# Kernel optimization log

Measured on AMD Instinct MI355X. Metric: run time of the kernel, lower is better.

## Reference

```python
import jax, jax.numpy as jnp
import numpy as np

SEG = 4  # segments


def setup_inputs() -> dict:
    key = jax.random.key(0)
    k1, k2, k3, k4 = jax.random.split(key, 4)
    B, C, H, W_ = 8, 64, 512, 512
    O = 64
    x = jax.random.normal(k1, (B, C, H, W_), dtype=jnp.float32)
    W = jax.random.normal(k2, (O, C), dtype=jnp.float32) * 0.05   # Linear weight [out, in]
    b = jax.random.normal(k3, (O,), dtype=jnp.float32) * 0.05
    seg_w = jax.random.normal(k4, (SEG, SEG), dtype=jnp.float32) * 0.1
    return {"x": x, "W": W, "b": b, "seg_w": seg_w}


def reference(x, W, b, seg_w):
    B, C, H, Wd = x.shape
    S = SEG
    hs, ws = H // S, Wd // S
    # segment mean-pool: [B, C, S, hs, S, ws] -> [B, C, S, S]
    pooled = x.reshape(B, C, S, hs, S, ws).mean(axis=(3, 5))
    # small linear per segment tile: [B, O, S, S]
    t = jnp.einsum('bcij,oc->boij', pooled, W) + b[None, :, None, None]
    weighted = t * seg_w[None, None, :, :]
    # broadcast each tile value back over its hs x ws block
    out = jnp.broadcast_to(
        weighted[:, :, :, None, :, None], (B, W.shape[0], S, hs, S, ws)
    ).reshape(B, W.shape[0], H, Wd)
    return out
```

## Files before the change

kernel.cpp:

```cpp
#include <hip/hip_runtime.h>

#define B_   8
#define C_   64
#define O_   64
#define H_   512
#define Wd_  512
#define SEG_ 4
#define HS_  128
#define WS_  128

__global__ __launch_bounds__(256) void pool_kernel(const float* __restrict__ x,
                                                   float* __restrict__ pooled) {
    const int blk = blockIdx.x;
    const int i   = blk & 3;
    const int bc  = blk >> 2;
    const float4* base =
        (const float4*)(x + ((size_t)bc * H_ + (size_t)i * HS_) * Wd_);

    const int tid = threadIdx.x;
    float sum = 0.f;
    #pragma unroll 8
    for (int f = tid; f < HS_ * Wd_ / 4; f += 256) {
        float4 v = base[f];
        sum += (v.x + v.y) + (v.z + v.w);
    }

    for (int off = 16; off >= 1; off >>= 1)
        sum += __shfl_down(sum, off, 32);

    __shared__ float sums[8];
    const int g = tid >> 5;
    if ((tid & 31) == 0) sums[g] = sum;
    __syncthreads();

    if (tid < 4) {
        float total = sums[tid] + sums[tid + 4];
        pooled[(size_t)blk * 4 + tid] = total * (1.0f / (HS_ * WS_));
    }
}

__global__ __launch_bounds__(256) void linear_kernel(const float* __restrict__ pooled,
                                                     const float* __restrict__ Wm,
                                                     const float* __restrict__ bias,
                                                     const float* __restrict__ seg_w,
                                                     float* __restrict__ weighted) {
    const int idx = blockIdx.x * 256 + threadIdx.x;
    if (idx >= B_ * O_ * 16) return;
    const int ij = idx & 15;
    const int o  = (idx >> 4) & (O_ - 1);
    const int b  = idx >> 10;

    const float* pp = pooled + (size_t)b * C_ * 16 + ij;
    const float* wr = Wm + (size_t)o * C_;
    float acc = 0.f;
    #pragma unroll 16
    for (int c = 0; c < C_; ++c)
        acc += pp[c * 16] * wr[c];

    weighted[idx] = (acc + bias[o]) * seg_w[ij];
}

__global__ __launch_bounds__(256) void bcast_kernel(const float* __restrict__ weighted,
                                                    float* __restrict__ out) {
    const int blk = blockIdx.x;
    const int i   = blk & 3;
    const int bo  = blk >> 2;
    const float* wv = weighted + (size_t)bo * 16 + (size_t)i * 4;

    const int tid = threadIdx.x;
    const int j   = (tid & 127) >> 5;
    const float v = wv[j];
    const float4 vv = make_float4(v, v, v, v);

    float4* base = (float4*)(out + ((size_t)bo * H_ + (size_t)i * HS_) * Wd_);
    #pragma unroll 8
    for (int f = tid; f < HS_ * Wd_ / 4; f += 256)
        base[f] = vv;
}

extern "C" void kernel_launch(void* const* d_in, const int* in_sizes, int n_in,
                              void* d_out, int out_size, void* d_ws, size_t ws_size,
                              hipStream_t stream) {
    const float* x     = (const float*)d_in[0];
    const float* Wm    = (const float*)d_in[1];
    const float* bias  = (const float*)d_in[2];
    const float* seg_w = (const float*)d_in[3];
    float* out = (float*)d_out;

    float* pooled   = (float*)d_ws;
    float* weighted = pooled + (size_t)B_ * C_ * 16;

    pool_kernel<<<B_ * C_ * SEG_, 256, 0, stream>>>(x, pooled);
    linear_kernel<<<(B_ * O_ * 16 + 255) / 256, 256, 0, stream>>>(
        pooled, Wm, bias, seg_w, weighted);
    bcast_kernel<<<B_ * O_ * SEG_, 256, 0, stream>>>(weighted, out);
}
```

Measured before the change: 865.9 us.

## Fuse linear into broadcast kernel and use nontemporal loads/stores

Merges the small linear kernel into the broadcast kernel. Each block computes its four tile values with a wave-wide shuffle reduction over the 64 channels and then writes its output region. Both the large input read and the large output write switch to nontemporal builtins so streaming data bypasses cache retention. This drops one kernel launch and the intermediate buffer, at the cost of each block redundantly recomputing a 64-term dot product.

```diff
diff --git a/kernel.cpp b/kernel.cpp
--- a/kernel.cpp
+++ b/kernel.cpp
@@ -9,19 +9,21 @@
 #define HS_  128
 #define WS_  128
 
+typedef float v4f __attribute__((ext_vector_type(4)));
+
 __global__ __launch_bounds__(256) void pool_kernel(const float* __restrict__ x,
                                                    float* __restrict__ pooled) {
     const int blk = blockIdx.x;
     const int i   = blk & 3;
     const int bc  = blk >> 2;
-    const float4* base =
-        (const float4*)(x + ((size_t)bc * H_ + (size_t)i * HS_) * Wd_);
+    const v4f* base =
+        (const v4f*)(x + ((size_t)bc * H_ + (size_t)i * HS_) * Wd_);
 
     const int tid = threadIdx.x;
     float sum = 0.f;
     #pragma unroll 8
     for (int f = tid; f < HS_ * Wd_ / 4; f += 256) {
-        float4 v = base[f];
+        v4f v = __builtin_nontemporal_load(&base[f]);
         sum += (v.x + v.y) + (v.z + v.w);
     }
 
@@ -39,43 +41,41 @@
     }
 }
 
-__global__ __launch_bounds__(256) void linear_kernel(const float* __restrict__ pooled,
-                                                     const float* __restrict__ Wm,
-                                                     const float* __restrict__ bias,
-                                                     const float* __restrict__ seg_w,
-                                                     float* __restrict__ weighted) {
-    const int idx = blockIdx.x * 256 + threadIdx.x;
-    if (idx >= B_ * O_ * 16) return;
-    const int ij = idx & 15;
-    const int o  = (idx >> 4) & (O_ - 1);
-    const int b  = idx >> 10;
-
-    const float* pp = pooled + (size_t)b * C_ * 16 + ij;
-    const float* wr = Wm + (size_t)o * C_;
-    float acc = 0.f;
-    #pragma unroll 16
-    for (int c = 0; c < C_; ++c)
-        acc += pp[c * 16] * wr[c];
-
-    weighted[idx] = (acc + bias[o]) * seg_w[ij];
-}
-
-__global__ __launch_bounds__(256) void bcast_kernel(const float* __restrict__ weighted,
-                                                    float* __restrict__ out) {
+__global__ __launch_bounds__(256) void linear_bcast_kernel(
+        const float* __restrict__ pooled,
+        const float* __restrict__ Wm,
+        const float* __restrict__ bias,
+        const float* __restrict__ seg_w,
+        float* __restrict__ out) {
     const int blk = blockIdx.x;
     const int i   = blk & 3;
     const int bo  = blk >> 2;
-    const float* wv = weighted + (size_t)bo * 16 + (size_t)i * 4;
+    const int o   = bo & (O_ - 1);
+    const int b   = bo >> 6;
 
-    const int tid = threadIdx.x;
-    const int j   = (tid & 127) >> 5;
-    const float v = wv[j];
-    const float4 vv = make_float4(v, v, v, v);
+    const int tid  = threadIdx.x;
+    const int wave = tid >> 6;
+    const int lane = tid & 63;
 
-    float4* base = (float4*)(out + ((size_t)bo * H_ + (size_t)i * HS_) * Wd_);
+    float partial = pooled[(size_t)b * C_ * 16 + lane * 16 + i * 4 + wave]
+                  * Wm[(size_t)o * C_ + lane];
+    #pragma unroll
+    for (int off = 32; off >= 1; off >>= 1)
+        partial += __shfl_down(partial, off, 64);
+
+    __shared__ float tile[4];
+    if (lane == 0)
+        tile[wave] = (partial + bias[o]) * seg_w[i * 4 + wave];
+    __syncthreads();
+
+    const float v = tile[(tid & 127) >> 5];
+    v4f vv;
+    vv.x = v; vv.y = v; vv.z = v; vv.w = v;
+
+    v4f* base = (v4f*)(out + ((size_t)bo * H_ + (size_t)i * HS_) * Wd_);
     #pragma unroll 8
     for (int f = tid; f < HS_ * Wd_ / 4; f += 256)
-        base[f] = vv;
+        __builtin_nontemporal_store(vv, &base[f]);
 }
 
 extern "C" void kernel_launch(void* const* d_in, const int* in_sizes, int n_in,
@@ -87,11 +87,9 @@
     const float* seg_w = (const float*)d_in[3];
     float* out = (float*)d_out;
 
-    float* pooled   = (float*)d_ws;
-    float* weighted = pooled + (size_t)B_ * C_ * 16;
+    float* pooled = (float*)d_ws;
 
     pool_kernel<<<B_ * C_ * SEG_, 256, 0, stream>>>(x, pooled);
-    linear_kernel<<<(B_ * O_ * 16 + 255) / 256, 256, 0, stream>>>(
-        pooled, Wm, bias, seg_w, weighted);
-    bcast_kernel<<<B_ * O_ * SEG_, 256, 0, stream>>>(weighted, out);
+    linear_bcast_kernel<<<B_ * O_ * SEG_, 256, 0, stream>>>(
+        pooled, Wm, bias, seg_w, out);
 }
```

Measured after the change: 820.4 us. 1.06x faster.
